# Performance work log

Hardware: AMD Instinct MI355X
Metric: run time of the kernel (lower is better)

## Reference

```python
import jax, jax.numpy as jnp
import numpy as np

B, S, D, FD = 2, 2048, 1024, 4096
EPS_LN = 1e-5


def _l2norm(x):
    n = jnp.linalg.norm(x, axis=-1, keepdims=True)
    return x / jnp.maximum(n, 1e-12)


def _layernorm(x, w, b):
    m = x.mean(-1, keepdims=True)
    v = ((x - m) ** 2).mean(-1, keepdims=True)
    return (x - m) / jnp.sqrt(v + EPS_LN) * w + b


def _spl(x, mu_w, mu_b, gate, proto):
    # cosine-similarity gated linear (SparseProtoLinear)
    scores = _l2norm(x) @ _l2norm(proto).T          # [..., out]
    rw = jax.nn.relu(scores - gate)
    comp = x @ mu_w.T + mu_b
    return comp * rw


def _rotate_half(x):
    h = x.shape[-1] // 2
    return jnp.concatenate([-x[..., h:], x[..., :h]], axis=-1)


def _forward(x, cos, sin,
             ln1_w, ln1_b, ln2_w, ln2_b,
             qkv_mu, qkv_proto, qkv_bias, qkv_gate,
             o_mu, o_proto, o_bias, o_gate,
             f1_mu, f1_proto, f1_bias, f1_gate,
             f2_mu, f2_proto, f2_bias, f2_gate,
             pt_qkv, pt_o, pt_f1, pt_f2,
             pln_qkv_w, pln_qkv_b, pln_o_w, pln_o_b,
             pln_f1_w, pln_f1_b, pln_f2_w, pln_f2_b,
             prev_qkv, prev_o, prev_f1, prev_f2):
    # effective protos: proto_weight + LN(Linear(prev_proto))
    eff_qkv = qkv_proto + _layernorm(prev_qkv @ pt_qkv.T, pln_qkv_w, pln_qkv_b)
    eff_o   = o_proto   + _layernorm(prev_o   @ pt_o.T,   pln_o_w,   pln_o_b)
    eff_f1  = f1_proto  + _layernorm(prev_f1  @ pt_f1.T,  pln_f1_w,  pln_f1_b)
    eff_f2  = f2_proto  + _layernorm(prev_f2  @ pt_f2.T,  pln_f2_w,  pln_f2_b)

    # attention
    attn_in = _layernorm(x, ln1_w, ln1_b)
    m_qkv = _spl(attn_in, qkv_mu, qkv_bias, qkv_gate, eff_qkv)   # [B,S,3D]
    q, k, v = jnp.split(m_qkv, 3, axis=-1)
    c = cos[None]; s = sin[None]
    q = q * c + _rotate_half(q) * s
    k = k * c + _rotate_half(k) * s
    scale = 1.0 / jnp.sqrt(jnp.asarray(D, x.dtype))
    scores = jnp.einsum('bqd,bkd->bqk', q, k) * scale            # [B,S,S]
    causal = jnp.tril(jnp.ones((S, S), dtype=bool))
    scores = jnp.where(causal[None], scores, jnp.finfo(x.dtype).min)
    attn = jax.nn.softmax(scores, axis=-1)
    attn_out = jnp.einsum('bqk,bkd->bqd', attn, v)
    m_o = _spl(attn_out, o_mu, o_bias, o_gate, eff_o)
    x1 = x + m_o

    # ffn (DynamicInfiniteExpert)
    ffn_in = _layernorm(x1, ln2_w, ln2_b)
    m1 = _spl(ffn_in, f1_mu, f1_bias, f1_gate, eff_f1)           # [B,S,FD]
    h = jax.nn.relu(m1)
    m2 = _spl(h, f2_mu, f2_bias, f2_gate, eff_f2)                # [B,S,D]
    return x1 + m2


def setup_inputs() -> dict:
    key = jax.random.key(0)
    ks = iter(jax.random.split(key, 64))

    def nrm(shape, scale=1.0):
        return jax.random.normal(next(ks), shape, dtype=jnp.float32) * scale

    # RoPE tables
    pos = np.arange(S, dtype=np.float32)
    inv_freq = 1.0 / (10000.0 ** (np.arange(0, D, 2, dtype=np.float32) / D))
    freqs = np.outer(pos, inv_freq)
    emb = np.concatenate([freqs, freqs], axis=-1)
    cos = jnp.asarray(np.cos(emb)); sin = jnp.asarray(np.sin(emb))

    sD = 1.0 / np.sqrt(D); sF = 1.0 / np.sqrt(FD)
    inp = {
        'x': nrm((B, S, D)), 'cos': cos, 'sin': sin,
        'ln1_w': jnp.ones((D,)), 'ln1_b': jnp.zeros((D,)),
        'ln2_w': jnp.ones((D,)), 'ln2_b': jnp.zeros((D,)),
        'qkv_mu': nrm((3 * D, D), sD), 'qkv_proto': nrm((3 * D, D), sD),
        'qkv_bias': jnp.zeros((3 * D,)), 'qkv_gate': jnp.zeros((3 * D,)),
        'o_mu': nrm((D, D), sD), 'o_proto': nrm((D, D), sD),
        'o_bias': jnp.zeros((D,)), 'o_gate': jnp.zeros((D,)),
        'f1_mu': nrm((FD, D), sD), 'f1_proto': nrm((FD, D), sD),
        'f1_bias': jnp.zeros((FD,)), 'f1_gate': jnp.zeros((FD,)),
        'f2_mu': nrm((D, FD), sF), 'f2_proto': nrm((D, FD), sF),
        'f2_bias': jnp.zeros((D,)), 'f2_gate': jnp.zeros((D,)),
        'pt_qkv': nrm((D, D), sD), 'pt_o': nrm((D, D), sD),
        'pt_f1': nrm((D, D), sD), 'pt_f2': nrm((FD, FD), sF),
        'pln_qkv_w': jnp.ones((D,)), 'pln_qkv_b': jnp.zeros((D,)),
        'pln_o_w': jnp.ones((D,)), 'pln_o_b': jnp.zeros((D,)),
        'pln_f1_w': jnp.ones((D,)), 'pln_f1_b': jnp.zeros((D,)),
        'pln_f2_w': jnp.ones((FD,)), 'pln_f2_b': jnp.zeros((FD,)),
        'prev_qkv': nrm((3 * D, D), sD), 'prev_o': nrm((D, D), sD),
        'prev_f1': nrm((FD, D), sD), 'prev_f2': nrm((D, FD), sF),
    }
    return inp


def reference(x, cos, sin,
              ln1_w, ln1_b, ln2_w, ln2_b,
              qkv_mu, qkv_proto, qkv_bias, qkv_gate,
              o_mu, o_proto, o_bias, o_gate,
              f1_mu, f1_proto, f1_bias, f1_gate,
              f2_mu, f2_proto, f2_bias, f2_gate,
              pt_qkv, pt_o, pt_f1, pt_f2,
              pln_qkv_w, pln_qkv_b, pln_o_w, pln_o_b,
              pln_f1_w, pln_f1_b, pln_f2_w, pln_f2_b,
              prev_qkv, prev_o, prev_f1, prev_f2):
    return _forward(x, cos, sin, ln1_w, ln1_b, ln2_w, ln2_b,
                    qkv_mu, qkv_proto, qkv_bias, qkv_gate,
                    o_mu, o_proto, o_bias, o_gate,
                    f1_mu, f1_proto, f1_bias, f1_gate,
                    f2_mu, f2_proto, f2_bias, f2_gate,
                    pt_qkv, pt_o, pt_f1, pt_f2,
                    pln_qkv_w, pln_qkv_b, pln_o_w, pln_o_b,
                    pln_f1_w, pln_f1_b, pln_f2_w, pln_f2_b,
                    prev_qkv, prev_o, prev_f1, prev_f2)
```

## Files before the change

### kernel.cpp

```cpp
#include <hip/hip_runtime.h>
#include <cstdint>

typedef unsigned short u16;
typedef __attribute__((ext_vector_type(8))) short sh8;
typedef __attribute__((ext_vector_type(4))) float f32x4;

struct __align__(8) us4 { u16 x, y, z, w; };

__device__ __forceinline__ u16 f2bf(float f) {
  unsigned u = __float_as_uint(f);
  u += 0x7FFFu + ((u >> 16) & 1u);
  return (u16)(u >> 16);
}
__device__ __forceinline__ float bf2f(u16 h) {
  return __uint_as_float((unsigned)h << 16);
}

__device__ __forceinline__ float blk_sum(float v, float* red) {
#pragma unroll
  for (int o = 32; o; o >>= 1) v += __shfl_xor(v, o);
  __syncthreads();
  if ((threadIdx.x & 63) == 0) red[threadIdx.x >> 6] = v;
  __syncthreads();
  return red[0] + red[1] + red[2] + red[3];
}
__device__ __forceinline__ float blk_max(float v, float* red) {
#pragma unroll
  for (int o = 32; o; o >>= 1) v = fmaxf(v, __shfl_xor(v, o));
  __syncthreads();
  if ((threadIdx.x & 63) == 0) red[threadIdx.x >> 6] = v;
  __syncthreads();
  return fmaxf(fmaxf(red[0], red[1]), fmaxf(red[2], red[3]));
}

__global__ void cvt_bf16(const float* __restrict__ S, u16* __restrict__ D, long n4) {
  long i = (long)blockIdx.x * blockDim.x + threadIdx.x;
  if (i >= n4) return;
  float4 v = ((const float4*)S)[i];
  us4 o; o.x = f2bf(v.x); o.y = f2bf(v.y); o.z = f2bf(v.z); o.w = f2bf(v.w);
  ((us4*)D)[i] = o;
}

__global__ void fillv(float* __restrict__ o, long n, float v) {
  long i = (long)blockIdx.x * blockDim.x + threadIdx.x;
  if (i < n) o[i] = v;
}

template <typename CT>
__global__ __launch_bounds__(256, 2) void gemm_bt(
    const u16* __restrict__ A, const u16* __restrict__ B, CT* __restrict__ C,
    int M, int N, int K, int lda, int ldb,
    int mode, long zsA, long zsB, long zsC) {
  int bm, bn;
  int z = blockIdx.z;
  if (mode == 3) {
    int t = blockIdx.x;
    int m = (int)floorf((sqrtf(8.f * t + 1.f) - 1.f) * 0.5f);
    while ((m + 1) * (m + 2) / 2 <= t) ++m;
    while (m * (m + 1) / 2 > t) --m;
    bm = m; bn = t - m * (m + 1) / 2;
  } else {
    bm = blockIdx.x; bn = blockIdx.y;
  }
  int k0s = 0, k0e = K;
  if (mode == 1) {
    int kc = K / gridDim.z;
    k0s = z * kc; k0e = k0s + kc;
    C += (size_t)z * M * (size_t)N;
  } else if (mode == 2 || mode == 3) {
    A += (size_t)z * zsA; B += (size_t)z * zsB; C += (size_t)z * zsC;
  } else if (mode == 4) {
    A += (size_t)z * zsA; B += (size_t)z * zsB; C += (size_t)z * zsC;
    k0e = (bm + 1) * 128;
  } else if (mode == 5) {
    int Mz = (int)((zsB >> (z * 16)) & 0xFFFF);
    if (bm * 128 >= Mz) return;
    A += (size_t)z * zsA; B += (size_t)z * 1048576; C += (size_t)z * zsC;
  }

  __shared__ __align__(16) u16 As[128 * 32];
  __shared__ __align__(16) u16 Bs[128 * 32];
  int tid = threadIdx.x, wid = tid >> 6, lane = tid & 63;
  int wr = (wid >> 1) << 6, wc = (wid & 1) << 6;
  int lr = lane & 15, lk = (lane >> 4) << 3;

  f32x4 acc[4][4];
  const f32x4 zf = {0.f, 0.f, 0.f, 0.f};
#pragma unroll
  for (int i = 0; i < 4; ++i)
#pragma unroll
    for (int j = 0; j < 4; ++j) acc[i][j] = zf;

  int r0 = tid >> 2, c0 = (tid & 3) << 3;
  const size_t baseA = (size_t)bm * 128, baseB = (size_t)bn * 128;
  const u16* Ab = A + baseA * lda;
  const u16* Bp = B + baseB * ldb;

  for (int k0 = k0s; k0 < k0e; k0 += 32) {
    __builtin_amdgcn_global_load_lds(
        (const __attribute__((address_space(1))) void*)(Ab + (size_t)r0 * lda + k0 + c0),
        (__attribute__((address_space(3))) void*)(As + (wid << 9)), 16, 0, 0);
    __builtin_amdgcn_global_load_lds(
        (const __attribute__((address_space(1))) void*)(Ab + (size_t)(64 + r0) * lda + k0 + c0),
        (__attribute__((address_space(3))) void*)(As + 2048 + (wid << 9)), 16, 0, 0);
    __builtin_amdgcn_global_load_lds(
        (const __attribute__((address_space(1))) void*)(Bp + (size_t)r0 * ldb + k0 + c0),
        (__attribute__((address_space(3))) void*)(Bs + (wid << 9)), 16, 0, 0);
    __builtin_amdgcn_global_load_lds(
        (const __attribute__((address_space(1))) void*)(Bp + (size_t)(64 + r0) * ldb + k0 + c0),
        (__attribute__((address_space(3))) void*)(Bs + 2048 + (wid << 9)), 16, 0, 0);
    __syncthreads();
    sh8 af[4], bfr[4];
#pragma unroll
    for (int f = 0; f < 4; ++f) {
      af[f]  = *(const sh8*)(As + (wr + f * 16 + lr) * 32 + lk);
      bfr[f] = *(const sh8*)(Bs + (wc + f * 16 + lr) * 32 + lk);
    }
#pragma unroll
    for (int i = 0; i < 4; ++i)
#pragma unroll
      for (int j = 0; j < 4; ++j)
        acc[i][j] = __builtin_amdgcn_mfma_f32_16x16x32_bf16(af[i], bfr[j], acc[i][j], 0, 0, 0);
    __syncthreads();
  }

  int cr = (lane >> 4) << 2, cc = lane & 15;
#pragma unroll
  for (int i = 0; i < 4; ++i)
#pragma unroll
    for (int j = 0; j < 4; ++j) {
      size_t cb = (baseA + wr + i * 16 + cr) * (size_t)N + (baseB + wc + j * 16 + cc);
#pragma unroll
      for (int r = 0; r < 4; ++r) {
        float v = acc[i][j][r];
        if constexpr (sizeof(CT) == 2) C[cb + (size_t)r * N] = (CT)f2bf(v);
        else                           C[cb + (size_t)r * N] = v;
      }
    }
}

__global__ void ln_rows(const float* __restrict__ X, const float* __restrict__ w,
                        const float* __restrict__ b, u16* __restrict__ Y,
                        float* __restrict__ norms, int C) {
  __shared__ float red[4];
  int row = blockIdx.x;
  const float* x = X + (size_t)row * C;
  int nv = C >> 2;
  float s = 0.f, ss = 0.f;
  for (int i = threadIdx.x; i < nv; i += 256) {
    float4 v = ((const float4*)x)[i];
    s += v.x + v.y + v.z + v.w;
    ss += v.x * v.x + v.y * v.y + v.z * v.z + v.w * v.w;
  }
  s = blk_sum(s, red);
  ss = blk_sum(ss, red);
  float mean = s / C;
  float inv = rsqrtf(fmaxf(ss / C - mean * mean, 0.f) + 1e-5f);
  float nrm = 0.f;
  for (int i = threadIdx.x; i < nv; i += 256) {
    float4 v = ((const float4*)x)[i];
    float4 wv = ((const float4*)w)[i];
    float4 bv = ((const float4*)b)[i];
    float y0 = (v.x - mean) * inv * wv.x + bv.x;
    float y1 = (v.y - mean) * inv * wv.y + bv.y;
    float y2 = (v.z - mean) * inv * wv.z + bv.z;
    float y3 = (v.w - mean) * inv * wv.w + bv.w;
    nrm += y0 * y0 + y1 * y1 + y2 * y2 + y3 * y3;
    us4 o; o.x = f2bf(y0); o.y = f2bf(y1); o.z = f2bf(y2); o.w = f2bf(y3);
    ((us4*)(Y + (size_t)row * C))[i] = o;
  }
  nrm = blk_sum(nrm, red);
  if (threadIdx.x == 0) norms[row] = fmaxf(sqrtf(nrm), 1e-12f);
}

__global__ void ln_add_norm(const u16* __restrict__ T0, const u16* __restrict__ T1,
                            const float* __restrict__ P,
                            const float* __restrict__ w, const float* __restrict__ b,
                            u16* __restrict__ E, float* __restrict__ norms, int C) {
  __shared__ float red[4];
  int row = blockIdx.x;
  const us4* t0 = (const us4*)(T0 + (size_t)row * C);
  const us4* t1 = T1 ? (const us4*)(T1 + (size_t)row * C) : nullptr;
  const float* p = P + (size_t)row * C;
  int nv = C >> 2;
  float s = 0.f, ss = 0.f;
  for (int i = threadIdx.x; i < nv; i += 256) {
    us4 v = t0[i];
    float f0 = bf2f(v.x), f1 = bf2f(v.y), f2 = bf2f(v.z), f3 = bf2f(v.w);
    if (t1) {
      us4 v1 = t1[i];
      f0 += bf2f(v1.x); f1 += bf2f(v1.y); f2 += bf2f(v1.z); f3 += bf2f(v1.w);
    }
    s += f0 + f1 + f2 + f3;
    ss += f0 * f0 + f1 * f1 + f2 * f2 + f3 * f3;
  }
  s = blk_sum(s, red);
  ss = blk_sum(ss, red);
  float mean = s / C;
  float inv = rsqrtf(fmaxf(ss / C - mean * mean, 0.f) + 1e-5f);
  float nrm = 0.f;
  for (int i = threadIdx.x; i < nv; i += 256) {
    us4 v = t0[i];
    float f0 = bf2f(v.x), f1 = bf2f(v.y), f2 = bf2f(v.z), f3 = bf2f(v.w);
    if (t1) {
      us4 v1 = t1[i];
      f0 += bf2f(v1.x); f1 += bf2f(v1.y); f2 += bf2f(v1.z); f3 += bf2f(v1.w);
    }
    float4 pv = ((const float4*)p)[i];
    float4 wv = ((const float4*)w)[i];
    float4 bv = ((const float4*)b)[i];
    float y0 = pv.x + (f0 - mean) * inv * wv.x + bv.x;
    float y1 = pv.y + (f1 - mean) * inv * wv.y + bv.y;
    float y2 = pv.z + (f2 - mean) * inv * wv.z + bv.z;
    float y3 = pv.w + (f3 - mean) * inv * wv.w + bv.w;
    nrm += y0 * y0 + y1 * y1 + y2 * y2 + y3 * y3;
    us4 o; o.x = f2bf(y0); o.y = f2bf(y1); o.z = f2bf(y2); o.w = f2bf(y3);
    ((us4*)(E + (size_t)row * C))[i] = o;
  }
  nrm = blk_sum(nrm, red);
  if (threadIdx.x == 0) norms[row] = fmaxf(sqrtf(nrm), 1e-12f);
}

__global__ void rownorm_bf(const u16* __restrict__ X, float* __restrict__ norms, int C) {
  __shared__ float red[4];
  int row = blockIdx.x;
  const us4* x = (const us4*)(X + (size_t)row * C);
  int nv = C >> 2;
  float nrm = 0.f;
  for (int i = threadIdx.x; i < nv; i += 256) {
    us4 v = x[i];
    float a = bf2f(v.x), b = bf2f(v.y), c = bf2f(v.z), d = bf2f(v.w);
    nrm += a * a + b * b + c * c + d * d;
  }
  nrm = blk_sum(nrm, red);
  if (threadIdx.x == 0) norms[row] = fmaxf(sqrtf(nrm), 1e-12f);
}

__device__ __forceinline__ void epi4(const u16* gr, int C, int c, float rr,
                                     const float* bias, const float* gate,
                                     const float* cn, float* o) {
  us4 cv = *(const us4*)(gr + c);
  us4 dv = *(const us4*)(gr + C + c);
  float4 bv = *(const float4*)(bias + c);
  float4 gv = *(const float4*)(gate + c);
  float4 nv = *(const float4*)(cn + c);
  float cf[4] = {bf2f(cv.x), bf2f(cv.y), bf2f(cv.z), bf2f(cv.w)};
  float df[4] = {bf2f(dv.x), bf2f(dv.y), bf2f(dv.z), bf2f(dv.w)};
  float bb[4] = {bv.x, bv.y, bv.z, bv.w};
  float gg[4] = {gv.x, gv.y, gv.z, gv.w};
  float nn[4] = {nv.x, nv.y, nv.z, nv.w};
#pragma unroll
  for (int j = 0; j < 4; ++j) {
    float sc = df[j] / (rr * nn[j]);
    o[j] = (cf[j] + bb[j]) * fmaxf(sc - gg[j], 0.f);
  }
}

__global__ void spl_rope_row(const u16* __restrict__ G, const float* __restrict__ bias,
                             const float* __restrict__ gate, const float* __restrict__ rn,
                             const float* __restrict__ cn, const float* __restrict__ CT_,
                             const float* __restrict__ ST_, u16* __restrict__ MQ) {
  int r = blockIdx.x;
  int s = r & 2047;
  const u16* gr = G + (size_t)r * 6144;
  u16* outr = MQ + (size_t)r * 3072;
  float rr = rn[r];
  int t = threadIdx.x;

  int qk = (t >> 7);
  int c = qk * 1024 + ((t & 127) << 2);
  int d = c - qk * 1024;
  float a0[4], a1[4];
  epi4(gr, 3072, c, rr, bias, gate, cn, a0);
  epi4(gr, 3072, c + 512, rr, bias, gate, cn, a1);
  const float* ct = CT_ + (size_t)s * 1024;
  const float* st = ST_ + (size_t)s * 1024;
  float4 c0 = *(const float4*)(ct + d);
  float4 s0 = *(const float4*)(st + d);
  float4 c1 = *(const float4*)(ct + d + 512);
  float4 s1 = *(const float4*)(st + d + 512);
  float cc0[4] = {c0.x, c0.y, c0.z, c0.w}, ss0[4] = {s0.x, s0.y, s0.z, s0.w};
  float cc1[4] = {c1.x, c1.y, c1.z, c1.w}, ss1[4] = {s1.x, s1.y, s1.z, s1.w};
  us4 o0, o1;
  o0.x = f2bf(a0[0] * cc0[0] - a1[0] * ss0[0]);
  o0.y = f2bf(a0[1] * cc0[1] - a1[1] * ss0[1]);
  o0.z = f2bf(a0[2] * cc0[2] - a1[2] * ss0[2]);
  o0.w = f2bf(a0[3] * cc0[3] - a1[3] * ss0[3]);
  o1.x = f2bf(a1[0] * cc1[0] + a0[0] * ss1[0]);
  o1.y = f2bf(a1[1] * cc1[1] + a0[1] * ss1[1]);
  o1.z = f2bf(a1[2] * cc1[2] + a0[2] * ss1[2]);
  o1.w = f2bf(a1[3] * cc1[3] + a0[3] * ss1[3]);
  *(us4*)(outr + c) = o0;
  *(us4*)(outr + c + 512) = o1;

  int cv_ = 2048 + (t << 2);
  float vv[4];
  epi4(gr, 3072, cv_, rr, bias, gate, cn, vv);
  us4 ov; ov.x = f2bf(vv[0]); ov.y = f2bf(vv[1]); ov.z = f2bf(vv[2]); ov.w = f2bf(vv[3]);
  *(us4*)(outr + cv_) = ov;
}

__global__ void spl_f1_row(const u16* __restrict__ G, const float* __restrict__ bias,
                           const float* __restrict__ gate, const float* __restrict__ rn,
                           const float* __restrict__ cn, u16* __restrict__ H,
                           float* __restrict__ rn_h) {
  __shared__ float red[4];
  int r = blockIdx.x;
  const u16* gr = G + (size_t)r * 8192;
  u16* hr = H + (size_t)r * 4096;
  float rr = rn[r];
  float nrm = 0.f;
  for (int c = threadIdx.x << 2; c < 4096; c += 1024) {
    float o[4];
    epi4(gr, 4096, c, rr, bias, gate, cn, o);
#pragma unroll
    for (int j = 0; j < 4; ++j) {
      o[j] = fmaxf(o[j], 0.f);
      nrm += o[j] * o[j];
    }
    us4 ov; ov.x = f2bf(o[0]); ov.y = f2bf(o[1]); ov.z = f2bf(o[2]); ov.w = f2bf(o[3]);
    *(us4*)(hr + c) = ov;
  }
  nrm = blk_sum(nrm, red);
  if (threadIdx.x == 0) rn_h[r] = fmaxf(sqrtf(nrm), 1e-12f);
}

__global__ void spl_o_ln_row(const u16* __restrict__ G, const float* __restrict__ bias,
                             const float* __restrict__ gate, const float* __restrict__ rn,
                             const float* __restrict__ cn, const float* __restrict__ xres,
                             const float* __restrict__ lw, const float* __restrict__ lb,
                             float* __restrict__ X1, u16* __restrict__ Y,
                             float* __restrict__ rn_ffn) {
  __shared__ float red[4];
  int r = blockIdx.x;
  int c = threadIdx.x << 2;
  const u16* gr = G + (size_t)r * 2048;
  float o[4];
  epi4(gr, 1024, c, rn[r], bias, gate, cn, o);
  float4 rv = *(const float4*)(xres + (size_t)r * 1024 + c);
  o[0] += rv.x; o[1] += rv.y; o[2] += rv.z; o[3] += rv.w;
  float4 xo = {o[0], o[1], o[2], o[3]};
  *(float4*)(X1 + (size_t)r * 1024 + c) = xo;
  float s = o[0] + o[1] + o[2] + o[3];
  float ss = o[0] * o[0] + o[1] * o[1] + o[2] * o[2] + o[3] * o[3];
  s = blk_sum(s, red);
  ss = blk_sum(ss, red);
  float mean = s * (1.f / 1024.f);
  float inv = rsqrtf(fmaxf(ss * (1.f / 1024.f) - mean * mean, 0.f) + 1e-5f);
  float4 wv = *(const float4*)(lw + c);
  float4 bv = *(const float4*)(lb + c);
  float ww[4] = {wv.x, wv.y, wv.z, wv.w}, bb[4] = {bv.x, bv.y, bv.z, bv.w};
  float nrm = 0.f;
  us4 ov;
  u16* op = (u16*)&ov;
#pragma unroll
  for (int j = 0; j < 4; ++j) {
    float y = (o[j] - mean) * inv * ww[j] + bb[j];
    nrm += y * y;
    op[j] = f2bf(y);
  }
  *(us4*)(Y + (size_t)r * 1024 + c) = ov;
  nrm = blk_sum(nrm, red);
  if (threadIdx.x == 0) rn_ffn[r] = fmaxf(sqrtf(nrm), 1e-12f);
}

__global__ void spl_epi_p(const u16* __restrict__ G0, const u16* __restrict__ G1,
                          const float* __restrict__ bias, const float* __restrict__ gate,
                          const float* __restrict__ rn, const float* __restrict__ cn,
                          const float* __restrict__ resid, float* __restrict__ out) {
  int r = blockIdx.x;
  int c = threadIdx.x << 2;
  size_t rowb = (size_t)r * 2048;
  us4 c0 = *(const us4*)(G0 + rowb + c);
  us4 c1 = *(const us4*)(G1 + rowb + c);
  us4 d0 = *(const us4*)(G0 + rowb + 1024 + c);
  us4 d1 = *(const us4*)(G1 + rowb + 1024 + c);
  float4 bv = *(const float4*)(bias + c);
  float4 gv = *(const float4*)(gate + c);
  float4 nv = *(const float4*)(cn + c);
  float4 rv = *(const float4*)(resid + (size_t)r * 1024 + c);
  float rr = rn[r];
  float cf[4] = {bf2f(c0.x) + bf2f(c1.x), bf2f(c0.y) + bf2f(c1.y),
                 bf2f(c0.z) + bf2f(c1.z), bf2f(c0.w) + bf2f(c1.w)};
  float df[4] = {bf2f(d0.x) + bf2f(d1.x), bf2f(d0.y) + bf2f(d1.y),
                 bf2f(d0.z) + bf2f(d1.z), bf2f(d0.w) + bf2f(d1.w)};
  float bb[4] = {bv.x, bv.y, bv.z, bv.w};
  float gg[4] = {gv.x, gv.y, gv.z, gv.w};
  float nn[4] = {nv.x, nv.y, nv.z, nv.w};
  float re[4] = {rv.x, rv.y, rv.z, rv.w};
  float4 ov;
  float* op = (float*)&ov;
#pragma unroll
  for (int j = 0; j < 4; ++j) {
    float sc = df[j] / (rr * nn[j]);
    op[j] = (cf[j] + bb[j]) * fmaxf(sc - gg[j], 0.f) + re[j];
  }
  *(float4*)(out + (size_t)r * 1024 + c) = ov;
}

__global__ void vtrans(const u16* __restrict__ MQ, u16* __restrict__ VT) {
  __shared__ u16 tile[32][33];
  int b = blockIdx.z;
  int s0 = blockIdx.x << 5, d0 = blockIdx.y << 5;
  int tx = threadIdx.x, ty = threadIdx.y;
  for (int r = ty; r < 32; r += 8)
    tile[r][tx] = MQ[((size_t)(b * 2048 + s0 + r)) * 3072 + 2048 + d0 + tx];
  __syncthreads();
  for (int r = ty; r < 32; r += 8)
    VT[(size_t)b * 1024 * 2048 + (size_t)(d0 + r) * 2048 + s0 + tx] = tile[tx][r];
}

__global__ void softmax_causal(const float* __restrict__ S, u16* __restrict__ P) {
  __shared__ float red[4];
  int b = blockIdx.x >> 11;
  int q = blockIdx.x & 2047;
  const float* row = S + ((size_t)b << 22) + (size_t)q * 2048;
  u16* prow = P + ((size_t)b << 22) + (size_t)q * 2048;
  int nv = q + 1;
  int wcap = ((q >> 7) + 1) << 7;
  int base = threadIdx.x * 8;
  float e[8];
  float m = -3.4e38f;
  float xv[8];
  bool live = base < nv;
  if (live) {
    float4 a = *(const float4*)(row + base);
    float4 bq = *(const float4*)(row + base + 4);
    xv[0] = a.x; xv[1] = a.y; xv[2] = a.z; xv[3] = a.w;
    xv[4] = bq.x; xv[5] = bq.y; xv[6] = bq.z; xv[7] = bq.w;
#pragma unroll
    for (int j = 0; j < 8; ++j) {
      xv[j] *= 0.03125f;
      if (base + j < nv) m = fmaxf(m, xv[j]);
    }
  }
  m = blk_max(m, red);
  float ssum = 0.f;
#pragma unroll
  for (int j = 0; j < 8; ++j) {
    e[j] = (live && base + j < nv) ? __expf(xv[j] - m) : 0.f;
    ssum += e[j];
  }
  ssum = blk_sum(ssum, red);
  float invs = 1.f / ssum;
  if (base < wcap) {
    us4 o;
    o.x = f2bf(e[0] * invs); o.y = f2bf(e[1] * invs);
    o.z = f2bf(e[2] * invs); o.w = f2bf(e[3] * invs);
    ((us4*)prow)[threadIdx.x * 2] = o;
    o.x = f2bf(e[4] * invs); o.y = f2bf(e[5] * invs);
    o.z = f2bf(e[6] * invs); o.w = f2bf(e[7] * invs);
    ((us4*)prow)[threadIdx.x * 2 + 1] = o;
  }
}

extern "C" void kernel_launch(void* const* d_in, const int* in_sizes, int n_in,
                              void* d_out, int out_size, void* d_ws, size_t ws_size,
                              hipStream_t stream) {
  (void)in_sizes;
  const float* x         = (const float*)d_in[0];
  const float* cosT      = (const float*)d_in[1];
  const float* sinT      = (const float*)d_in[2];
  const float* ln1_w     = (const float*)d_in[3];
  const float* ln1_b     = (const float*)d_in[4];
  const float* ln2_w     = (const float*)d_in[5];
  const float* ln2_b     = (const float*)d_in[6];
  const float* qkv_mu    = (const float*)d_in[7];
  const float* qkv_proto = (const float*)d_in[8];
  const float* qkv_bias  = (const float*)d_in[9];
  const float* qkv_gate  = (const float*)d_in[10];
  const float* o_mu      = (const float*)d_in[11];
  const float* o_proto   = (const float*)d_in[12];
  const float* o_bias    = (const float*)d_in[13];
  const float* o_gate    = (const float*)d_in[14];
  const float* f1_mu     = (const float*)d_in[15];
  const float* f1_proto  = (const float*)d_in[16];
  const float* f1_bias   = (const float*)d_in[17];
  const float* f1_gate   = (const float*)d_in[18];
  const float* f2_mu     = (const float*)d_in[19];
  const float* f2_proto  = (const float*)d_in[20];
  const float* f2_bias   = (const float*)d_in[21];
  const float* f2_gate   = (const float*)d_in[22];
  const float* pt_qkv    = (const float*)d_in[23];
  const float* pt_o      = (const float*)d_in[24];
  const float* pt_f1     = (const float*)d_in[25];
  const float* pt_f2     = (const float*)d_in[26];
  const float* pln_qkv_w = (const float*)d_in[27];
  const float* pln_qkv_b = (const float*)d_in[28];
  const float* pln_o_w   = (const float*)d_in[29];
  const float* pln_o_b   = (const float*)d_in[30];
  const float* pln_f1_w  = (const float*)d_in[31];
  const float* pln_f1_b  = (const float*)d_in[32];
  const float* pln_f2_w  = (const float*)d_in[33];
  const float* pln_f2_b  = (const float*)d_in[34];
  const float* prev_qkv  = (const float*)d_in[35];
  const float* prev_o    = (const float*)d_in[36];
  const float* prev_f1   = (const float*)d_in[37];
  const float* prev_f2   = (const float*)d_in[38];

  const long D = 1024, TD = 3072, FD = 4096, R = 4096;

  char* W = (char*)d_ws;
  size_t off = 0;
  auto alloc = [&](size_t bytes) {
    void* p = W + off;
    off = (off + bytes + 255) & ~(size_t)255;
    return p;
  };
  char* GOUT = (char*)alloc(67108864);
  u16*  RC   = (u16*)alloc(33554432);
  u16*  wq   = (u16*)alloc(2 * TD * D * 2);
  u16*  wo   = (u16*)alloc(2 * D * D * 2);
  u16*  wf1  = (u16*)alloc(2 * FD * D * 2);
  u16*  wf2  = (u16*)alloc(2 * D * FD * 2);
  float* X1  = (float*)alloc(R * D * 4);
  u16*  P1   = (u16*)alloc(R * D * 2);
  u16*  VT   = (u16*)alloc(2 * D * 2048 * 2);
  u16*  AOB  = (u16*)alloc(R * D * 2);
  float* pnq     = (float*)alloc(TD * 4);
  float* pno     = (float*)alloc(D * 4);
  float* pnf1    = (float*)alloc(FD * 4);
  float* pnf2    = (float*)alloc(D * 4);
  float* rn_ain  = (float*)alloc(R * 4);
  float* rn_aout = (float*)alloc(R * 4);
  float* rn_ffn  = (float*)alloc(R * 4);
  float* rn_h    = (float*)alloc(R * 4);
  size_t need = off;

  if (n_in < 39 || need > ws_size) {
    long n = out_size;
    fillv<<<dim3((unsigned)((n + 255) / 256)), 256, 0, stream>>>((float*)d_out, n, 12345.0f);
    return;
  }

  u16* SA = (u16*)GOUT;
  u16* SB = (u16*)(GOUT + 25165824);
  float* SCORES = (float*)GOUT;
  u16* PB = (u16*)(GOUT + 33554432);

  auto cvt = [&](const float* s, u16* d, long n) {
    long n4 = n >> 2;
    cvt_bf16<<<dim3((unsigned)((n4 + 255) / 256)), 256, 0, stream>>>(s, d, n4);
  };

  cvt(prev_f1,  SA,            FD * D);
  cvt(prev_qkv, SA + 4194304,  TD * D);
  cvt(prev_o,   SA + 8388608,  D * D);
  cvt(pt_f1,    SB,            D * D);
  cvt(pt_qkv,   SB + 1048576,  D * D);
  cvt(pt_o,     SB + 2097152,  D * D);
  {
    long Mz = 4096L | (3072L << 16) | (1024L << 32);
    gemm_bt<u16><<<dim3(32, 8, 3), 256, 0, stream>>>(
        SA, SB, RC, 4096, 1024, 1024, 1024, 1024, 5, 4194304, Mz, 4194304);
  }
  ln_add_norm<<<4096, 256, 0, stream>>>(RC, nullptr, f1_proto, pln_f1_w, pln_f1_b,
                                        wf1 + (size_t)FD * D, pnf1, 1024);
  ln_add_norm<<<3072, 256, 0, stream>>>(RC + 4194304, nullptr, qkv_proto, pln_qkv_w,
                                        pln_qkv_b, wq + (size_t)TD * D, pnq, 1024);
  ln_add_norm<<<1024, 256, 0, stream>>>(RC + 8388608, nullptr, o_proto, pln_o_w,
                                        pln_o_b, wo + (size_t)D * D, pno, 1024);
  cvt(prev_f2, SA, D * FD);
  cvt(pt_f2,   SB, (long)FD * FD);
  gemm_bt<u16><<<dim3(8, 32, 2), 256, 0, stream>>>(
      SA, SB, RC, 1024, 4096, 4096, 4096, 4096, 1, 0, 0, 0);
  ln_add_norm<<<1024, 256, 0, stream>>>(RC, RC + 4194304, f2_proto, pln_f2_w, pln_f2_b,
                                        wf2 + (size_t)D * FD, pnf2, 4096);
  cvt(qkv_mu, wq, TD * D);
  cvt(o_mu,   wo, D * D);
  cvt(f1_mu,  wf1, FD * D);
  cvt(f2_mu,  wf2, D * FD);

  ln_rows<<<4096, 256, 0, stream>>>(x, ln1_w, ln1_b, P1, rn_ain, 1024);
  gemm_bt<u16><<<dim3(32, 48, 1), 256, 0, stream>>>(
      P1, wq, (u16*)GOUT, 4096, 6144, 1024, 1024, 1024, 0, 0, 0, 0);
  spl_rope_row<<<4096, 256, 0, stream>>>(
      (u16*)GOUT, qkv_bias, qkv_gate, rn_ain, pnq, cosT, sinT, RC);

  vtrans<<<dim3(64, 32, 2), dim3(32, 8), 0, stream>>>(RC, VT);
  gemm_bt<float><<<dim3(136, 1, 2), 256, 0, stream>>>(
      RC, RC + 1024, SCORES, 2048, 2048, 1024, 3072, 3072,
      3, 2048L * 3072, 2048L * 3072, 1L << 22);
  softmax_causal<<<4096, 256, 0, stream>>>(SCORES, PB);
  gemm_bt<u16><<<dim3(16, 8, 2), 256, 0, stream>>>(
      PB, VT, AOB, 2048, 1024, 2048, 2048, 2048,
      4, 1L << 22, 1024L * 2048, 2048L * 1024);
  rownorm_bf<<<4096, 256, 0, stream>>>(AOB, rn_aout, 1024);

  gemm_bt<u16><<<dim3(32, 16, 1), 256, 0, stream>>>(
      AOB, wo, (u16*)GOUT, 4096, 2048, 1024, 1024, 1024, 0, 0, 0, 0);
  spl_o_ln_row<<<4096, 256, 0, stream>>>(
      (u16*)GOUT, o_bias, o_gate, rn_aout, pno, x, ln2_w, ln2_b, X1, P1, rn_ffn);

  gemm_bt<u16><<<dim3(32, 64, 1), 256, 0, stream>>>(
      P1, wf1, (u16*)GOUT, 4096, 8192, 1024, 1024, 1024, 0, 0, 0, 0);
  spl_f1_row<<<4096, 256, 0, stream>>>(
      (u16*)GOUT, f1_bias, f1_gate, rn_ffn, pnf1, RC, rn_h);
  gemm_bt<u16><<<dim3(32, 16, 2), 256, 0, stream>>>(
      RC, wf2, (u16*)GOUT, 4096, 2048, 4096, 4096, 4096, 1, 0, 0, 0);
  spl_epi_p<<<4096, 256, 0, stream>>>(
      (u16*)GOUT, (u16*)GOUT + 8388608, f2_bias, f2_gate, rn_h, pnf2,
      X1, (float*)d_out);
}
```

Measured before the change: 596.0 us.

## Add 256x256 multi-stage pipelined GEMM for QKV and FFN projections

Introduces a new gemm256 kernel with 512 threads, 256x256 output tiles and a 4-stage LDS ring buffer. The ring is filled with async global_load_lds and gated by explicit vmcnt waits, and reads go through an XOR-swizzled LDS layout to avoid bank conflicts. It replaces the 128x128 single-buffered gemm_bt for the QKV, FFN1 and split-K FFN2 projections, aiming to raise data reuse and overlap loads with MFMA work. In exchange it needs 128 KB of dynamic LDS with one block per CU, and the large tiles can leave the last wave of blocks only partly filling the CUs.

```diff
diff --git a/kernel.cpp b/kernel.cpp
--- a/kernel.cpp
+++ b/kernel.cpp
@@ -44,6 +44,126 @@
 __global__ void fillv(float* __restrict__ o, long n, float v) {
   long i = (long)blockIdx.x * blockDim.x + threadIdx.x;
   if (i < n) o[i] = v;
+}
+
+#define GL16(gp, lp)                                                        \
+  __builtin_amdgcn_global_load_lds(                                         \
+      (const __attribute__((address_space(1))) void*)(gp),                  \
+      (__attribute__((address_space(3))) void*)(lp), 16, 0, 0)
+
+template <typename CT>
+__global__ __launch_bounds__(512, 1) void gemm256(
+    const u16* __restrict__ A, const u16* __restrict__ B, CT* __restrict__ C,
+    int M, int N, int K, int lda, int ldb, int kchunk) {
+  extern __shared__ u16 lds[];
+  int tid = threadIdx.x;
+  int wid = tid >> 6, lane = tid & 63;
+  int wm = wid >> 2, wn = wid & 3;
+  int bm = blockIdx.x, bn = blockIdx.y;
+  int k0s = 0, nt;
+  if (kchunk) {
+    k0s = blockIdx.z * kchunk;
+    C += (size_t)blockIdx.z * M * (size_t)N;
+    nt = kchunk >> 5;
+  } else {
+    nt = K >> 5;
+  }
+  const size_t baseArow = (size_t)bm * 256;
+  const size_t baseBrow = (size_t)bn * 256;
+
+  int ci = (wid << 6) + lane;
+  int rowS = ci >> 2;
+  int kcS = (ci ^ (ci >> 3)) & 3;
+  const u16* gA0 = A + (baseArow + rowS) * lda + k0s + kcS * 8;
+  const u16* gA1 = gA0 + (size_t)128 * lda;
+  const u16* gB0 = B + (baseBrow + rowS) * ldb + k0s + kcS * 8;
+  const u16* gB1 = gB0 + (size_t)128 * ldb;
+  u16* dBase = lds + (wid << 9);
+
+  int l15 = lane & 15, l4 = lane >> 4;
+  int aoff[8], boff[4];
+#pragma unroll
+  for (int fr = 0; fr < 8; ++fr) {
+    int by = (wm * 128 + fr * 16 + l15) * 64 + l4 * 16;
+    aoff[fr] = (by ^ (((by >> 7) & 3) << 4)) >> 1;
+  }
+#pragma unroll
+  for (int fc = 0; fc < 4; ++fc) {
+    int by = (wn * 64 + fc * 16 + l15) * 64 + l4 * 16;
+    boff[fc] = 8192 + ((by ^ (((by >> 7) & 3) << 4)) >> 1);
+  }
+
+  f32x4 acc[8][4];
+  const f32x4 zf = {0.f, 0.f, 0.f, 0.f};
+#pragma unroll
+  for (int i = 0; i < 8; ++i)
+#pragma unroll
+    for (int j = 0; j < 4; ++j) acc[i][j] = zf;
+
+#define STAGE256(ts)                                                  \
+  do {                                                                \
+    int ss_ = (ts) & 3;                                               \
+    int kk_ = (ts) << 5;                                              \
+    u16* d_ = dBase + ss_ * 16384;                                    \
+    GL16(gA0 + kk_, d_);                                              \
+    GL16(gA1 + kk_, d_ + 4096);                                       \
+    GL16(gB0 + kk_, d_ + 8192);                                       \
+    GL16(gB1 + kk_, d_ + 12288);                                      \
+  } while (0)
+
+  STAGE256(0);
+  STAGE256(1);
+  STAGE256(2);
+  asm volatile("s_waitcnt vmcnt(8)" ::: "memory");
+  __builtin_amdgcn_s_barrier();
+  __builtin_amdgcn_sched_barrier(0);
+
+  for (int t = 0; t < nt; ++t) {
+    int ts = t + 3;
+    if (ts < nt) STAGE256(ts);
+
+    const u16* sl = lds + (t & 3) * 16384;
+    sh8 af[8], bfv[4];
+#pragma unroll
+    for (int fc = 0; fc < 4; ++fc) bfv[fc] = *(const sh8*)(sl + boff[fc]);
+#pragma unroll
+    for (int fr = 0; fr < 8; ++fr) af[fr] = *(const sh8*)(sl + aoff[fr]);
+
+    __builtin_amdgcn_s_setprio(1);
+#pragma unroll
+    for (int fr = 0; fr < 8; ++fr)
+#pragma unroll
+      for (int fc = 0; fc < 4; ++fc)
+        acc[fr][fc] = __builtin_amdgcn_mfma_f32_16x16x32_bf16(af[fr], bfv[fc],
+                                                              acc[fr][fc], 0, 0, 0);
+    __builtin_amdgcn_s_setprio(0);
+
+    int rem = nt - 2 - t;
+    if (rem >= 2)      asm volatile("s_waitcnt vmcnt(8)" ::: "memory");
+    else if (rem == 1) asm volatile("s_waitcnt vmcnt(4)" ::: "memory");
+    else if (rem == 0) asm volatile("s_waitcnt vmcnt(0)" ::: "memory");
+    if (t < nt - 1) {
+      __builtin_amdgcn_s_barrier();
+      __builtin_amdgcn_sched_barrier(0);
+    }
+  }
+#undef STAGE256
+
+  int cr = l4 << 2, cc = l15;
+  const size_t rbase = baseArow + wm * 128 + cr;
+  const size_t cbase = baseBrow + wn * 64 + cc;
+#pragma unroll
+  for (int fr = 0; fr < 8; ++fr)
+#pragma unroll
+    for (int fc = 0; fc < 4; ++fc) {
+      size_t cb = (rbase + fr * 16) * (size_t)N + cbase + fc * 16;
+#pragma unroll
+      for (int r = 0; r < 4; ++r) {
+        float v = acc[fr][fc][r];
+        if constexpr (sizeof(CT) == 2) C[cb + (size_t)r * N] = (CT)f2bf(v);
+        else                           C[cb + (size_t)r * N] = v;
+      }
+    }
 }
 
 template <typename CT>
@@ -97,18 +217,10 @@
   const u16* Bp = B + baseB * ldb;
 
   for (int k0 = k0s; k0 < k0e; k0 += 32) {
-    __builtin_amdgcn_global_load_lds(
-        (const __attribute__((address_space(1))) void*)(Ab + (size_t)r0 * lda + k0 + c0),
-        (__attribute__((address_space(3))) void*)(As + (wid << 9)), 16, 0, 0);
-    __builtin_amdgcn_global_load_lds(
-        (const __attribute__((address_space(1))) void*)(Ab + (size_t)(64 + r0) * lda + k0 + c0),
-        (__attribute__((address_space(3))) void*)(As + 2048 + (wid << 9)), 16, 0, 0);
-    __builtin_amdgcn_global_load_lds(
-        (const __attribute__((address_space(1))) void*)(Bp + (size_t)r0 * ldb + k0 + c0),
-        (__attribute__((address_space(3))) void*)(Bs + (wid << 9)), 16, 0, 0);
-    __builtin_amdgcn_global_load_lds(
-        (const __attribute__((address_space(1))) void*)(Bp + (size_t)(64 + r0) * ldb + k0 + c0),
-        (__attribute__((address_space(3))) void*)(Bs + 2048 + (wid << 9)), 16, 0, 0);
+    GL16(Ab + (size_t)r0 * lda + k0 + c0, As + (wid << 9));
+    GL16(Ab + (size_t)(64 + r0) * lda + k0 + c0, As + 2048 + (wid << 9));
+    GL16(Bp + (size_t)r0 * ldb + k0 + c0, Bs + (wid << 9));
+    GL16(Bp + (size_t)(64 + r0) * ldb + k0 + c0, Bs + 2048 + (wid << 9));
     __syncthreads();
     sh8 af[4], bfr[4];
 #pragma unroll
@@ -572,8 +684,8 @@
   cvt(f2_mu,  wf2, D * FD);
 
   ln_rows<<<4096, 256, 0, stream>>>(x, ln1_w, ln1_b, P1, rn_ain, 1024);
-  gemm_bt<u16><<<dim3(32, 48, 1), 256, 0, stream>>>(
-      P1, wq, (u16*)GOUT, 4096, 6144, 1024, 1024, 1024, 0, 0, 0, 0);
+  gemm256<u16><<<dim3(16, 24), 512, 131072, stream>>>(
+      P1, wq, (u16*)GOUT, 4096, 6144, 1024, 1024, 1024, 0);
   spl_rope_row<<<4096, 256, 0, stream>>>(
       (u16*)GOUT, qkv_bias, qkv_gate, rn_ain, pnq, cosT, sinT, RC);
 
@@ -592,12 +704,12 @@
   spl_o_ln_row<<<4096, 256, 0, stream>>>(
       (u16*)GOUT, o_bias, o_gate, rn_aout, pno, x, ln2_w, ln2_b, X1, P1, rn_ffn);
 
-  gemm_bt<u16><<<dim3(32, 64, 1), 256, 0, stream>>>(
-      P1, wf1, (u16*)GOUT, 4096, 8192, 1024, 1024, 1024, 0, 0, 0, 0);
+  gemm256<u16><<<dim3(16, 32), 512, 131072, stream>>>(
+      P1, wf1, (u16*)GOUT, 4096, 8192, 1024, 1024, 1024, 0);
   spl_f1_row<<<4096, 256, 0, stream>>>(
       (u16*)GOUT, f1_bias, f1_gate, rn_ffn, pnf1, RC, rn_h);
-  gemm_bt<u16><<<dim3(32, 16, 2), 256, 0, stream>>>(
-      RC, wf2, (u16*)GOUT, 4096, 2048, 4096, 4096, 4096, 1, 0, 0, 0);
+  gemm256<u16><<<dim3(16, 8, 2), 512, 131072, stream>>>(
+      RC, wf2, (u16*)GOUT, 4096, 2048, 4096, 4096, 4096, 2048);
   spl_epi_p<<<4096, 256, 0, stream>>>(
       (u16*)GOUT, (u16*)GOUT + 8388608, f2_bias, f2_gate, rn_h, pnf2,
       X1, (float*)d_out);
```

Result: no change. 589.7 us (-1.1%).

## Add 256x256 pipelined GEMM with fused SPL epilogue via interleaved weight layout

Applied to the files above, without the earlier changes.

Adds a 512-thread 256x256-tile GEMM with a 4-stage global-to-LDS pipeline and swizzled LDS layout. The mu and proto weight rows are interleaved (stride 2048) so each output column pair holds the comp and dot values, which lets the SPL gating epilogue run inside the GEMM and write half-width output directly. This replaces the separate spl_rope_row and spl_f1_row passes with a small in-place RoPE kernel and a row-norm kernel, and the f2 GEMM moves to the new kernel with a split-K of two. The large tiles mean fewer blocks per GEMM, which risks underfilling the GPU, and the epilogue adds cross-lane shuffles.

```diff
diff --git a/kernel.cpp b/kernel.cpp
--- a/kernel.cpp
+++ b/kernel.cpp
@@ -41,9 +41,170 @@
   ((us4*)D)[i] = o;
 }
 
+__global__ void cvt_str(const float* __restrict__ S, u16* __restrict__ Dst,
+                        int K, long ostride) {
+  int row = blockIdx.x;
+  const float* s = S + (size_t)row * K;
+  u16* d = Dst + (size_t)row * ostride;
+  for (int c = threadIdx.x << 2; c < K; c += 1024) {
+    float4 v = *(const float4*)(s + c);
+    us4 o; o.x = f2bf(v.x); o.y = f2bf(v.y); o.z = f2bf(v.z); o.w = f2bf(v.w);
+    *(us4*)(d + c) = o;
+  }
+}
+
 __global__ void fillv(float* __restrict__ o, long n, float v) {
   long i = (long)blockIdx.x * blockDim.x + threadIdx.x;
   if (i < n) o[i] = v;
+}
+
+#define GL16(gp, lp)                                                        \
+  __builtin_amdgcn_global_load_lds(                                         \
+      (const __attribute__((address_space(1))) void*)(gp),                  \
+      (__attribute__((address_space(3))) void*)(lp), 16, 0, 0)
+
+#define G256_PROLOG()                                                          \
+  extern __shared__ u16 lds[];                                                 \
+  int tid = threadIdx.x;                                                       \
+  int wid = tid >> 6, lane = tid & 63;                                         \
+  int wm = wid >> 2, wn = wid & 3;                                             \
+  int bm = blockIdx.x, bn = blockIdx.y;                                        \
+  int k0s = 0, nt;                                                             \
+  if (kchunk) {                                                                \
+    k0s = blockIdx.z * kchunk;                                                 \
+    nt = kchunk >> 5;                                                          \
+  } else {                                                                     \
+    nt = K >> 5;                                                               \
+  }                                                                            \
+  const size_t baseArow = (size_t)bm * 256;                                    \
+  const size_t baseBrow = (size_t)bn * 256;                                    \
+  int ci = (wid << 6) + lane;                                                  \
+  int rowS = ci >> 2;                                                          \
+  int kcS = (ci ^ (ci >> 3)) & 3;                                              \
+  const u16* gA0 = A + (baseArow + rowS) * lda + k0s + kcS * 8;                \
+  const u16* gA1 = gA0 + (size_t)128 * lda;                                    \
+  const u16* gB0 = B + (baseBrow + rowS) * ldb + k0s + kcS * 8;                \
+  const u16* gB1 = gB0 + (size_t)128 * ldb;                                    \
+  u16* dBase = lds + (wid << 9);                                               \
+  int l15 = lane & 15, l4 = lane >> 4;                                         \
+  int aoff[8], boff[4];                                                        \
+  _Pragma("unroll") for (int fr = 0; fr < 8; ++fr) {                           \
+    int by = (wm * 128 + fr * 16 + l15) * 64 + l4 * 16;                        \
+    aoff[fr] = (by ^ (((by >> 7) & 3) << 4)) >> 1;                             \
+  }                                                                            \
+  _Pragma("unroll") for (int fc = 0; fc < 4; ++fc) {                           \
+    int by = (wn * 64 + fc * 16 + l15) * 64 + l4 * 16;                         \
+    boff[fc] = 8192 + ((by ^ (((by >> 7) & 3) << 4)) >> 1);                    \
+  }                                                                            \
+  f32x4 acc[8][4];                                                             \
+  const f32x4 zf = {0.f, 0.f, 0.f, 0.f};                                       \
+  _Pragma("unroll") for (int i = 0; i < 8; ++i)                                \
+    _Pragma("unroll") for (int j = 0; j < 4; ++j) acc[i][j] = zf;
+
+#define STAGE256(ts)                                                  \
+  do {                                                                \
+    int ss_ = (ts) & 3;                                               \
+    int kk_ = (ts) << 5;                                              \
+    u16* d_ = dBase + ss_ * 16384;                                    \
+    GL16(gA0 + kk_, d_);                                              \
+    GL16(gA1 + kk_, d_ + 4096);                                       \
+    GL16(gB0 + kk_, d_ + 8192);                                       \
+    GL16(gB1 + kk_, d_ + 12288);                                      \
+  } while (0)
+
+#define G256_KLOOP()                                                           \
+  STAGE256(0);                                                                 \
+  STAGE256(1);                                                                 \
+  STAGE256(2);                                                                 \
+  asm volatile("s_waitcnt vmcnt(8)" ::: "memory");                             \
+  __builtin_amdgcn_s_barrier();                                                \
+  __builtin_amdgcn_sched_barrier(0);                                           \
+  for (int t = 0; t < nt; ++t) {                                               \
+    int ts = t + 3;                                                            \
+    if (ts < nt) STAGE256(ts);                                                 \
+    const u16* sl = lds + (t & 3) * 16384;                                     \
+    sh8 af[8], bfv[4];                                                         \
+    _Pragma("unroll") for (int fc = 0; fc < 4; ++fc)                           \
+        bfv[fc] = *(const sh8*)(sl + boff[fc]);                                \
+    _Pragma("unroll") for (int fr = 0; fr < 8; ++fr)                           \
+        af[fr] = *(const sh8*)(sl + aoff[fr]);                                 \
+    __builtin_amdgcn_s_setprio(1);                                             \
+    _Pragma("unroll") for (int fr = 0; fr < 8; ++fr)                           \
+      _Pragma("unroll") for (int fc = 0; fc < 4; ++fc)                         \
+        acc[fr][fc] = __builtin_amdgcn_mfma_f32_16x16x32_bf16(                 \
+            af[fr], bfv[fc], acc[fr][fc], 0, 0, 0);                            \
+    __builtin_amdgcn_s_setprio(0);                                             \
+    int rem = nt - 2 - t;                                                      \
+    if (rem >= 2)      asm volatile("s_waitcnt vmcnt(8)" ::: "memory");        \
+    else if (rem == 1) asm volatile("s_waitcnt vmcnt(4)" ::: "memory");        \
+    else if (rem == 0) asm volatile("s_waitcnt vmcnt(0)" ::: "memory");        \
+    if (t < nt - 1) {                                                          \
+      __builtin_amdgcn_s_barrier();                                            \
+      __builtin_amdgcn_sched_barrier(0);                                       \
+    }                                                                          \
+  }
+
+template <typename CT>
+__global__ __launch_bounds__(512, 1) void gemm256(
+    const u16* __restrict__ A, const u16* __restrict__ B, CT* __restrict__ C,
+    int M, int N, int K, int lda, int ldb, int kchunk) {
+  if (kchunk) C += (size_t)blockIdx.z * M * (size_t)N;
+  G256_PROLOG();
+  G256_KLOOP();
+  int cr = l4 << 2, cc = l15;
+  const size_t rbase = baseArow + wm * 128 + cr;
+  const size_t cbase = baseBrow + wn * 64 + cc;
+#pragma unroll
+  for (int fr = 0; fr < 8; ++fr)
+#pragma unroll
+    for (int fc = 0; fc < 4; ++fc) {
+      size_t cb = (rbase + fr * 16) * (size_t)N + cbase + fc * 16;
+#pragma unroll
+      for (int r = 0; r < 4; ++r) {
+        float v = acc[fr][fc][r];
+        if constexpr (sizeof(CT) == 2) C[cb + (size_t)r * N] = (CT)f2bf(v);
+        else                           C[cb + (size_t)r * N] = v;
+      }
+    }
+}
+
+__global__ __launch_bounds__(512, 1) void gemm256_spl(
+    const u16* __restrict__ A, const u16* __restrict__ B, u16* __restrict__ out,
+    int M, int N, int K, int lda, int ldb, int kchunk,
+    const float* __restrict__ bias, const float* __restrict__ gate,
+    const float* __restrict__ rn, const float* __restrict__ cn, int relu_out) {
+  G256_PROLOG();
+  G256_KLOOP();
+  int cr = l4 << 2, cc = l15;
+  const size_t rbase = baseArow + wm * 128 + cr;
+  const size_t cbase = baseBrow + wn * 64 + cc;
+  const int F = N >> 1;
+  bool evenL = (cc & 1) == 0;
+  float bb[4], gg[4], nn[4];
+  int ft[4];
+#pragma unroll
+  for (int fc = 0; fc < 4; ++fc) {
+    ft[fc] = (int)((cbase + fc * 16) >> 1);
+    bb[fc] = bias[ft[fc]]; gg[fc] = gate[ft[fc]]; nn[fc] = cn[ft[fc]];
+  }
+#pragma unroll
+  for (int fr = 0; fr < 8; ++fr)
+#pragma unroll
+    for (int r = 0; r < 4; ++r) {
+      size_t row = rbase + fr * 16 + r;
+      float rr = rn[row];
+#pragma unroll
+      for (int fc = 0; fc < 4; ++fc) {
+        float mine = acc[fr][fc][r];
+        float other = __shfl_xor(mine, 1);
+        float comp = evenL ? mine : other;
+        float dots = evenL ? other : mine;
+        float sc = dots / (rr * nn[fc]);
+        float v = (comp + bb[fc]) * fmaxf(sc - gg[fc], 0.f);
+        if (relu_out) v = fmaxf(v, 0.f);
+        if (evenL) out[row * (size_t)F + ft[fc]] = f2bf(v);
+      }
+    }
 }
 
 template <typename CT>
@@ -97,18 +258,10 @@
   const u16* Bp = B + baseB * ldb;
 
   for (int k0 = k0s; k0 < k0e; k0 += 32) {
-    __builtin_amdgcn_global_load_lds(
-        (const __attribute__((address_space(1))) void*)(Ab + (size_t)r0 * lda + k0 + c0),
-        (__attribute__((address_space(3))) void*)(As + (wid << 9)), 16, 0, 0);
-    __builtin_amdgcn_global_load_lds(
-        (const __attribute__((address_space(1))) void*)(Ab + (size_t)(64 + r0) * lda + k0 + c0),
-        (__attribute__((address_space(3))) void*)(As + 2048 + (wid << 9)), 16, 0, 0);
-    __builtin_amdgcn_global_load_lds(
-        (const __attribute__((address_space(1))) void*)(Bp + (size_t)r0 * ldb + k0 + c0),
-        (__attribute__((address_space(3))) void*)(Bs + (wid << 9)), 16, 0, 0);
-    __builtin_amdgcn_global_load_lds(
-        (const __attribute__((address_space(1))) void*)(Bp + (size_t)(64 + r0) * ldb + k0 + c0),
-        (__attribute__((address_space(3))) void*)(Bs + 2048 + (wid << 9)), 16, 0, 0);
+    GL16(Ab + (size_t)r0 * lda + k0 + c0, As + (wid << 9));
+    GL16(Ab + (size_t)(64 + r0) * lda + k0 + c0, As + 2048 + (wid << 9));
+    GL16(Bp + (size_t)r0 * ldb + k0 + c0, Bs + (wid << 9));
+    GL16(Bp + (size_t)(64 + r0) * ldb + k0 + c0, Bs + 2048 + (wid << 9));
     __syncthreads();
     sh8 af[4], bfr[4];
 #pragma unroll
@@ -176,7 +329,8 @@
 __global__ void ln_add_norm(const u16* __restrict__ T0, const u16* __restrict__ T1,
                             const float* __restrict__ P,
                             const float* __restrict__ w, const float* __restrict__ b,
-                            u16* __restrict__ E, float* __restrict__ norms, int C) {
+                            u16* __restrict__ E, float* __restrict__ norms, int C,
+                            long ostride) {
   __shared__ float red[4];
   int row = blockIdx.x;
   const us4* t0 = (const us4*)(T0 + (size_t)row * C);
@@ -215,7 +369,7 @@
     float y3 = pv.w + (f3 - mean) * inv * wv.w + bv.w;
     nrm += y0 * y0 + y1 * y1 + y2 * y2 + y3 * y3;
     us4 o; o.x = f2bf(y0); o.y = f2bf(y1); o.z = f2bf(y2); o.w = f2bf(y3);
-    ((us4*)(E + (size_t)row * C))[i] = o;
+    *(us4*)(E + (size_t)row * ostride + (i << 2)) = o;
   }
   nrm = blk_sum(nrm, red);
   if (threadIdx.x == 0) norms[row] = fmaxf(sqrtf(nrm), 1e-12f);
@@ -256,73 +410,21 @@
   }
 }
 
-__global__ void spl_rope_row(const u16* __restrict__ G, const float* __restrict__ bias,
-                             const float* __restrict__ gate, const float* __restrict__ rn,
-                             const float* __restrict__ cn, const float* __restrict__ CT_,
-                             const float* __restrict__ ST_, u16* __restrict__ MQ) {
-  int r = blockIdx.x;
-  int s = r & 2047;
-  const u16* gr = G + (size_t)r * 6144;
-  u16* outr = MQ + (size_t)r * 3072;
-  float rr = rn[r];
-  int t = threadIdx.x;
-
-  int qk = (t >> 7);
-  int c = qk * 1024 + ((t & 127) << 2);
-  int d = c - qk * 1024;
-  float a0[4], a1[4];
-  epi4(gr, 3072, c, rr, bias, gate, cn, a0);
-  epi4(gr, 3072, c + 512, rr, bias, gate, cn, a1);
-  const float* ct = CT_ + (size_t)s * 1024;
-  const float* st = ST_ + (size_t)s * 1024;
-  float4 c0 = *(const float4*)(ct + d);
-  float4 s0 = *(const float4*)(st + d);
-  float4 c1 = *(const float4*)(ct + d + 512);
-  float4 s1 = *(const float4*)(st + d + 512);
-  float cc0[4] = {c0.x, c0.y, c0.z, c0.w}, ss0[4] = {s0.x, s0.y, s0.z, s0.w};
-  float cc1[4] = {c1.x, c1.y, c1.z, c1.w}, ss1[4] = {s1.x, s1.y, s1.z, s1.w};
-  us4 o0, o1;
-  o0.x = f2bf(a0[0] * cc0[0] - a1[0] * ss0[0]);
-  o0.y = f2bf(a0[1] * cc0[1] - a1[1] * ss0[1]);
-  o0.z = f2bf(a0[2] * cc0[2] - a1[2] * ss0[2]);
-  o0.w = f2bf(a0[3] * cc0[3] - a1[3] * ss0[3]);
-  o1.x = f2bf(a1[0] * cc1[0] + a0[0] * ss1[0]);
-  o1.y = f2bf(a1[1] * cc1[1] + a0[1] * ss1[1]);
-  o1.z = f2bf(a1[2] * cc1[2] + a0[2] * ss1[2]);
-  o1.w = f2bf(a1[3] * cc1[3] + a0[3] * ss1[3]);
-  *(us4*)(outr + c) = o0;
-  *(us4*)(outr + c + 512) = o1;
-
-  int cv_ = 2048 + (t << 2);
-  float vv[4];
-  epi4(gr, 3072, cv_, rr, bias, gate, cn, vv);
-  us4 ov; ov.x = f2bf(vv[0]); ov.y = f2bf(vv[1]); ov.z = f2bf(vv[2]); ov.w = f2bf(vv[3]);
-  *(us4*)(outr + cv_) = ov;
-}
-
-__global__ void spl_f1_row(const u16* __restrict__ G, const float* __restrict__ bias,
-                           const float* __restrict__ gate, const float* __restrict__ rn,
-                           const float* __restrict__ cn, u16* __restrict__ H,
-                           float* __restrict__ rn_h) {
-  __shared__ float red[4];
-  int r = blockIdx.x;
-  const u16* gr = G + (size_t)r * 8192;
-  u16* hr = H + (size_t)r * 4096;
-  float rr = rn[r];
-  float nrm = 0.f;
-  for (int c = threadIdx.x << 2; c < 4096; c += 1024) {
-    float o[4];
-    epi4(gr, 4096, c, rr, bias, gate, cn, o);
-#pragma unroll
-    for (int j = 0; j < 4; ++j) {
-      o[j] = fmaxf(o[j], 0.f);
-      nrm += o[j] * o[j];
-    }
-    us4 ov; ov.x = f2bf(o[0]); ov.y = f2bf(o[1]); ov.z = f2bf(o[2]); ov.w = f2bf(o[3]);
-    *(us4*)(hr + c) = ov;
-  }
-  nrm = blk_sum(nrm, red);
-  if (threadIdx.x == 0) rn_h[r] = fmaxf(sqrtf(nrm), 1e-12f);
+__global__ void rope_ip(u16* __restrict__ MQ, const float* __restrict__ CT_,
+                        const float* __restrict__ ST_) {
+  long t = (long)blockIdx.x * blockDim.x + threadIdx.x;
+  int i = (int)(t & 511);
+  long row = t >> 9;
+  int s = (int)(row & 2047);
+  u16* base = MQ + row * 3072;
+  float c0 = CT_[(size_t)s * 1024 + i], c1 = CT_[(size_t)s * 1024 + 512 + i];
+  float s0 = ST_[(size_t)s * 1024 + i], s1 = ST_[(size_t)s * 1024 + 512 + i];
+  float q0 = bf2f(base[i]), q1 = bf2f(base[512 + i]);
+  base[i]        = f2bf(q0 * c0 - q1 * s0);
+  base[512 + i]  = f2bf(q1 * c1 + q0 * s1);
+  float k0 = bf2f(base[1024 + i]), k1 = bf2f(base[1536 + i]);
+  base[1024 + i] = f2bf(k0 * c0 - k1 * s0);
+  base[1536 + i] = f2bf(k1 * c1 + k0 * s1);
 }
 
 __global__ void spl_o_ln_row(const u16* __restrict__ G, const float* __restrict__ bias,
@@ -555,27 +657,27 @@
         SA, SB, RC, 4096, 1024, 1024, 1024, 1024, 5, 4194304, Mz, 4194304);
   }
   ln_add_norm<<<4096, 256, 0, stream>>>(RC, nullptr, f1_proto, pln_f1_w, pln_f1_b,
-                                        wf1 + (size_t)FD * D, pnf1, 1024);
+                                        wf1 + 1024, pnf1, 1024, 2048);
   ln_add_norm<<<3072, 256, 0, stream>>>(RC + 4194304, nullptr, qkv_proto, pln_qkv_w,
-                                        pln_qkv_b, wq + (size_t)TD * D, pnq, 1024);
+                                        pln_qkv_b, wq + 1024, pnq, 1024, 2048);
   ln_add_norm<<<1024, 256, 0, stream>>>(RC + 8388608, nullptr, o_proto, pln_o_w,
-                                        pln_o_b, wo + (size_t)D * D, pno, 1024);
+                                        pln_o_b, wo + (size_t)D * D, pno, 1024, 1024);
   cvt(prev_f2, SA, D * FD);
   cvt(pt_f2,   SB, (long)FD * FD);
   gemm_bt<u16><<<dim3(8, 32, 2), 256, 0, stream>>>(
       SA, SB, RC, 1024, 4096, 4096, 4096, 4096, 1, 0, 0, 0);
   ln_add_norm<<<1024, 256, 0, stream>>>(RC, RC + 4194304, f2_proto, pln_f2_w, pln_f2_b,
-                                        wf2 + (size_t)D * FD, pnf2, 4096);
-  cvt(qkv_mu, wq, TD * D);
+                                        wf2 + (size_t)D * FD, pnf2, 4096, 4096);
+  cvt_str<<<3072, 256, 0, stream>>>(qkv_mu, wq, 1024, 2048);
+  cvt_str<<<4096, 256, 0, stream>>>(f1_mu, wf1, 1024, 2048);
   cvt(o_mu,   wo, D * D);
-  cvt(f1_mu,  wf1, FD * D);
   cvt(f2_mu,  wf2, D * FD);
 
   ln_rows<<<4096, 256, 0, stream>>>(x, ln1_w, ln1_b, P1, rn_ain, 1024);
-  gemm_bt<u16><<<dim3(32, 48, 1), 256, 0, stream>>>(
-      P1, wq, (u16*)GOUT, 4096, 6144, 1024, 1024, 1024, 0, 0, 0, 0);
-  spl_rope_row<<<4096, 256, 0, stream>>>(
-      (u16*)GOUT, qkv_bias, qkv_gate, rn_ain, pnq, cosT, sinT, RC);
+  gemm256_spl<<<dim3(16, 24), 512, 131072, stream>>>(
+      P1, wq, RC, 4096, 6144, 1024, 1024, 1024, 0,
+      qkv_bias, qkv_gate, rn_ain, pnq, 0);
+  rope_ip<<<dim3((unsigned)((R * 512) / 256)), 256, 0, stream>>>(RC, cosT, sinT);
 
   vtrans<<<dim3(64, 32, 2), dim3(32, 8), 0, stream>>>(RC, VT);
   gemm_bt<float><<<dim3(136, 1, 2), 256, 0, stream>>>(
@@ -592,12 +694,12 @@
   spl_o_ln_row<<<4096, 256, 0, stream>>>(
       (u16*)GOUT, o_bias, o_gate, rn_aout, pno, x, ln2_w, ln2_b, X1, P1, rn_ffn);
 
-  gemm_bt<u16><<<dim3(32, 64, 1), 256, 0, stream>>>(
-      P1, wf1, (u16*)GOUT, 4096, 8192, 1024, 1024, 1024, 0, 0, 0, 0);
-  spl_f1_row<<<4096, 256, 0, stream>>>(
-      (u16*)GOUT, f1_bias, f1_gate, rn_ffn, pnf1, RC, rn_h);
-  gemm_bt<u16><<<dim3(32, 16, 2), 256, 0, stream>>>(
-      RC, wf2, (u16*)GOUT, 4096, 2048, 4096, 4096, 4096, 1, 0, 0, 0);
+  gemm256_spl<<<dim3(16, 32), 512, 131072, stream>>>(
+      P1, wf1, RC, 4096, 8192, 1024, 1024, 1024, 0,
+      f1_bias, f1_gate, rn_ffn, pnf1, 1);
+  rownorm_bf<<<4096, 256, 0, stream>>>(RC, rn_h, 4096);
+  gemm256<u16><<<dim3(16, 8, 2), 512, 131072, stream>>>(
+      RC, wf2, (u16*)GOUT, 4096, 2048, 4096, 4096, 4096, 2048);
   spl_epi_p<<<4096, 256, 0, stream>>>(
       (u16*)GOUT, (u16*)GOUT + 8388608, f2_bias, f2_gate, rn_h, pnf2,
       X1, (float*)d_out);
```

Measured after the change: 636.4 us. +6.8%, slower.
